# Kernel tuning notes

Measured on AMD Instinct MI355X. Metric: run time of the kernel, lower is better.

Reference implementation:

```python
import jax, jax.numpy as jnp
import numpy as np

B, R, L = 1024, 10, 512  # batch, num_rounds, lstm_size
EPS = 1e-10


def _gated(x, Wy, by, Wg, bg):
    # GatedTrans: tanh(Linear(x)) * sigmoid(Linear(x)); dropout is identity in eval
    return jnp.tanh(x @ Wy + by) * jax.nn.sigmoid(x @ Wg + bg)


def setup_inputs() -> dict:
    key = jax.random.key(0)
    ks = jax.random.split(key, 16)
    s_in = 1.0 / np.sqrt(2 * L)
    s_hid = 1.0 / np.sqrt(L)
    inp = {
        "hist": jax.random.normal(ks[0], (B, R, 2 * L), jnp.float32),
        "ques": jax.random.normal(ks[1], (B, R, 2 * L), jnp.float32),
        "noise": jax.random.uniform(ks[2], (B, R, R), jnp.float32),
        # H_embed GatedTrans params
        "Wy_h": jax.random.normal(ks[3], (2 * L, L), jnp.float32) * s_in,
        "by_h": jnp.zeros((L,), jnp.float32),
        "Wg_h": jax.random.normal(ks[4], (2 * L, L), jnp.float32) * s_in,
        "bg_h": jnp.zeros((L,), jnp.float32),
        # Q_embed GatedTrans params
        "Wy_q": jax.random.normal(ks[5], (2 * L, L), jnp.float32) * s_in,
        "by_q": jnp.zeros((L,), jnp.float32),
        "Wg_q": jax.random.normal(ks[6], (2 * L, L), jnp.float32) * s_in,
        "bg_q": jnp.zeros((L,), jnp.float32),
        # MLP: Linear(2L->L), Linear(L->1)
        "W1": jax.random.normal(ks[7], (2 * L, L), jnp.float32) * s_in,
        "b1": jnp.zeros((L,), jnp.float32),
        "W2": jax.random.normal(ks[8], (L, 1), jnp.float32) * s_hid,
        "b2": jnp.zeros((1,), jnp.float32),
        # att: Linear(2->1)
        "Wa": jax.random.normal(ks[9], (2, 1), jnp.float32) * 0.7,
        "ba": jnp.zeros((1,), jnp.float32),
    }
    return inp


def _forward(hist, ques, noise, Wy_h, by_h, Wg_h, bg_h, Wy_q, by_q, Wg_q, bg_q,
             W1, b1, W2, b2, Wa, ba):
    h = _gated(hist, Wy_h, by_h, Wg_h, bg_h)  # [B,R,L], indexed by j (history round)
    q = _gated(ques, Wy_q, by_q, Wg_q, bg_q)  # [B,R,L], indexed by i (question round)
    # MLP layer 1 on concat(h_j, q_i) without materializing the 2L concat:
    sh = h @ W1[:L] + b1            # [B,R,L] (j part + bias)
    sq = q @ W1[L:]                 # [B,R,L] (i part)
    hid = sq[:, :, None, :] + sh[:, None, :, :]  # [B,R(i),R(j),L]
    score = (hid @ W2 + b2)[..., 0]              # [B,R,R]
    # delta_t = cumsum over rows of lower-triangular ones
    tri = jnp.tril(jnp.ones((R, R), jnp.float32))
    delta_t = jnp.cumsum(tri, axis=0)            # [R,R]
    # att Linear(2->1) on concat(score, delta_t)
    logits = score * Wa[0, 0] + delta_t * Wa[1, 0] + ba[0]  # [B,R,R]
    # per-round Gumbel softmax over prefix [:i+1], vectorized with tril mask
    g = -jnp.log(EPS - jnp.log(noise + EPS))     # Gumbel(0,1) noise
    mask = tri.astype(bool)                       # [R,R], True for j<=i
    z = jnp.where(mask, logits + g, -1e9)
    y_soft = jax.nn.softmax(z, axis=-1)           # temperature = 1
    one_hot = jax.nn.one_hot(jnp.argmax(z, axis=-1), R, dtype=logits.dtype)
    # straight-through: value = one_hot, gradient flows through y_soft (valid cols only)
    y = one_hot + (y_soft - jax.lax.stop_gradient(y_soft)) * tri
    return y


def reference(hist, ques, noise, Wy_h, by_h, Wg_h, bg_h, Wy_q, by_q, Wg_q, bg_q,
              W1, b1, W2, b2, Wa, ba):
    return _forward(hist, ques, noise, Wy_h, by_h, Wg_h, bg_h, Wy_q, by_q,
                    Wg_q, bg_q, W1, b1, W2, b2, Wa, ba)
```

## Files before the change

### kernel.cpp

```cpp
#include <hip/hip_runtime.h>
#include <math.h>

typedef float f4 __attribute__((ext_vector_type(4)));
typedef float f32x4 __attribute__((ext_vector_type(4)));
typedef _Float16 h4 __attribute__((ext_vector_type(4)));
typedef _Float16 h8 __attribute__((ext_vector_type(8)));

#define NB 1024
#define NR 10
#define NL 512
#define NM (NB*NR)
#define NK (2*NL)

#define BIMG_OFF   131072ull
#define BIMG_EMBED 4194304ull
#define WS_NEED    (BIMG_OFF + 2ull*BIMG_EMBED)

#define SCALE_A 16.0f
#define SCALE_B 512.0f
#define INV_SCALE (1.0f/8192.0f)

__global__ __launch_bounds__(256) void k_init(float* __restrict__ t) {
    int i = blockIdx.x*256 + threadIdx.x;
    if (i < 2*NM) t[i] = 0.0f;
}

__global__ __launch_bounds__(256) void k_vcalc(const float* __restrict__ W1,
                                               const float* __restrict__ b1,
                                               const float* __restrict__ W2,
                                               const float* __restrict__ b2,
                                               float* __restrict__ vh,
                                               float* __restrict__ vq,
                                               float* __restrict__ cc) {
    int tid = blockIdx.x*256 + threadIdx.x;
    if (tid < 2*NL) {
        const float* row = W1 + (size_t)tid*NL;
        float s = 0.0f;
        #pragma unroll 4
        for (int k = 0; k < NL; ++k) s = fmaf(row[k], W2[k], s);
        if (tid < NL) vh[tid] = s; else vq[tid-NL] = s;
    } else if (tid == 2*NL) {
        float s = 0.0f;
        for (int k = 0; k < NL; ++k) s = fmaf(b1[k], W2[k], s);
        cc[0] = s + b2[0];
    }
}

__global__ __launch_bounds__(256) void k_wsplit(const float* __restrict__ Wy_h,
    const float* __restrict__ Wg_h, const float* __restrict__ Wy_q,
    const float* __restrict__ Wg_q, char* __restrict__ Bimg)
{
    const int nh = blockIdx.x;
    const int ks = blockIdx.y;
    const int mi = blockIdx.z;
    const float* W = (mi==0) ? Wy_h : (mi==1) ? Wg_h : (mi==2) ? Wy_q : Wg_q;
    const int emb = mi >> 1, nfb = (mi & 1) * 4;
    __shared__ float Ws[32][68];
    const int t = threadIdx.x;
    const int kl = t >> 4, nl4 = (t & 15) * 4;
    #pragma unroll
    for (int i = 0; i < 2; ++i) {
        f4 wv = *(const f4*)(W + (size_t)(ks*32 + kl + 16*i)*NL + nh*64 + nl4);
        *(f4*)&Ws[kl + 16*i][nl4] = wv;
    }
    __syncthreads();
    const int kg = t >> 6, nl = t & 63;
    h8 hi, lo;
    #pragma unroll
    for (int e8 = 0; e8 < 8; ++e8) {
        float x = Ws[kg*8 + e8][nl] * SCALE_B;
        _Float16 h = (_Float16)x;
        hi[e8] = h;
        lo[e8] = (_Float16)(x - (float)h);
    }
    const int nf  = nfb + (nl >> 4);
    const int l16 = (nl & 15) + 16*kg;
    char* p = Bimg + (size_t)emb*BIMG_EMBED
            + ((size_t)(nh*32 + ks)*2)*8192 + nf*1024 + l16*16;
    *(h8*)p = hi;
    *(h8*)(p + 8192) = lo;
}

__global__ __launch_bounds__(256, 2) void k_embed_mfma(
    const float* __restrict__ hist, const float* __restrict__ ques,
    const char* __restrict__ Bimg,
    const float* __restrict__ by_h, const float* __restrict__ bg_h,
    const float* __restrict__ by_q, const float* __restrict__ bg_q,
    const float* __restrict__ vv,
    float* __restrict__ tout)
{
    const int z = blockIdx.z;
    const float* X  = z ? ques : hist;
    const float* by = z ? by_q : by_h;
    const float* bg = z ? bg_q : bg_h;
    const float* v  = vv + z*NL;
    float* tptr = tout + (size_t)z*NM;
    const int nt = blockIdx.y;
    const char* Bt0 = Bimg + (size_t)z*BIMG_EMBED + (size_t)nt*32*16384;
    const int row0 = blockIdx.x * 128;

    __shared__ uint4 smem[2048];
    char* sA = (char*)smem;
    char* sB = sA + 16384;
    uint4* sB4 = smem + 1024;

    const int t = threadIdx.x;
    const int l = t & 63, w = t >> 6;
    const int wr = w >> 1, wc = w & 1;

    const int arow = t >> 3;
    const int ak4  = (t & 7) << 2;
    const int akg  = (t & 7) >> 1;
    const int ae0  = (t & 1) << 2;
    const float* Xp = X + (size_t)(row0 + arow)*NK + ak4;
    const int awb = ((arow >> 4) * 1024) + (((arow & 15) + 16*akg) * 16) + ae0*2;

    f32x4 acc[4][4];
    #pragma unroll
    for (int m = 0; m < 4; ++m)
      #pragma unroll
      for (int n = 0; n < 4; ++n) { f32x4 zz = {0.f,0.f,0.f,0.f}; acc[m][n] = zz; }

    for (int ks = 0; ks < 32; ++ks) {
        const int k0 = ks << 5;
        #pragma unroll
        for (int i = 0; i < 4; ++i) {
            f4 a = *(const f4*)(Xp + k0 + (size_t)i*32*NK);
            h4 hi, lo;
            #pragma unroll
            for (int j = 0; j < 4; ++j) {
                float xs = a[j] * SCALE_A;
                _Float16 h = (_Float16)xs;
                hi[j] = h;
                lo[j] = (_Float16)(xs - (float)h);
            }
            *(h4*)(sA +        awb + i*2048) = hi;
            *(h4*)(sA + 8192 + awb + i*2048) = lo;
        }
        const uint4* bt = (const uint4*)(Bt0 + (size_t)ks*16384);
        #pragma unroll
        for (int j = 0; j < 4; ++j) sB4[t + 256*j] = bt[t + 256*j];
        __syncthreads();
        h8 av[4][2], bv[4][2];
        #pragma unroll
        for (int m = 0; m < 4; ++m)
          #pragma unroll
          for (int s = 0; s < 2; ++s)
            av[m][s] = *(const h8*)(sA + s*8192 + (wr*4 + m)*1024 + l*16);
        #pragma unroll
        for (int fn = 0; fn < 4; ++fn) {
            const int nf = (fn < 2) ? (wc*2 + fn) : (4 + wc*2 + (fn - 2));
            #pragma unroll
            for (int s = 0; s < 2; ++s)
                bv[fn][s] = *(const h8*)(sB + s*8192 + nf*1024 + l*16);
        }
        #pragma unroll
        for (int m = 0; m < 4; ++m)
          #pragma unroll
          for (int fn = 0; fn < 4; ++fn) {
            acc[m][fn] = __builtin_amdgcn_mfma_f32_16x16x32_f16(av[m][0], bv[fn][0], acc[m][fn], 0, 0, 0);
            acc[m][fn] = __builtin_amdgcn_mfma_f32_16x16x32_f16(av[m][0], bv[fn][1], acc[m][fn], 0, 0, 0);
            acc[m][fn] = __builtin_amdgcn_mfma_f32_16x16x32_f16(av[m][1], bv[fn][0], acc[m][fn], 0, 0, 0);
          }
        __syncthreads();
    }

    const int coll = l & 15, rg = l >> 4;
    #pragma unroll
    for (int m = 0; m < 4; ++m) {
      #pragma unroll
      for (int r = 0; r < 4; ++r) {
        float ps = 0.0f;
        #pragma unroll
        for (int n = 0; n < 2; ++n) {
            const int c = nt*64 + wc*32 + n*16 + coll;
            float y = acc[m][n  ][r]*INV_SCALE + by[c];
            float g = acc[m][n+2][r]*INV_SCALE + bg[c];
            ps += v[c] * (tanhf(y) * (1.0f/(1.0f + expf(-g))));
        }
        ps += __shfl_xor(ps, 1);
        ps += __shfl_xor(ps, 2);
        ps += __shfl_xor(ps, 4);
        ps += __shfl_xor(ps, 8);
        if (coll == 0)
            atomicAdd(&tptr[row0 + wr*64 + m*16 + rg*4 + r], ps);
      }
    }
}

__global__ __launch_bounds__(256) void k_embed(const float* __restrict__ X,
    const float* __restrict__ Wy, const float* __restrict__ by,
    const float* __restrict__ Wg, const float* __restrict__ bg,
    const float* __restrict__ v, float* __restrict__ tout)
{
    __shared__ float As[32][68];
    __shared__ float Bys[32][64];
    __shared__ float Bgs[32][64];
    const int tid  = threadIdx.x;
    const int row0 = blockIdx.x * 64;
    const int c0   = blockIdx.y * 64;
    const int tx = tid & 15, ty = tid >> 4;
    float accy[4][4] = {};
    float accg[4][4] = {};
    const int arow = tid >> 3;
    const int ak   = (tid & 7) << 2;
    const int bk   = tid >> 4;
    const int bc   = (tid & 15) << 2;
    const float* Xp0 = X + (size_t)(row0 + arow)*NK + ak;
    const float* Xp1 = Xp0 + (size_t)32*NK;
    for (int k0 = 0; k0 < NK; k0 += 32) {
        f4 a0 = *(const f4*)(Xp0 + k0);
        f4 a1 = *(const f4*)(Xp1 + k0);
        f4 y0 = *(const f4*)&Wy[(size_t)(k0+bk   )*NL + c0 + bc];
        f4 y1 = *(const f4*)&Wy[(size_t)(k0+bk+16)*NL + c0 + bc];
        f4 g0 = *(const f4*)&Wg[(size_t)(k0+bk   )*NL + c0 + bc];
        f4 g1 = *(const f4*)&Wg[(size_t)(k0+bk+16)*NL + c0 + bc];
        #pragma unroll
        for (int j = 0; j < 4; ++j) {
            As[ak+j][arow]      = a0[j];
            As[ak+j][arow + 32] = a1[j];
        }
        *(f4*)&Bys[bk   ][bc] = y0;
        *(f4*)&Bys[bk+16][bc] = y1;
        *(f4*)&Bgs[bk   ][bc] = g0;
        *(f4*)&Bgs[bk+16][bc] = g1;
        __syncthreads();
        #pragma unroll
        for (int kk = 0; kk < 32; ++kk) {
            f4 a   = *(const f4*)&As [kk][ty<<2];
            f4 byv = *(const f4*)&Bys[kk][tx<<2];
            f4 bgv = *(const f4*)&Bgs[kk][tx<<2];
            #pragma unroll
            for (int rr = 0; rr < 4; ++rr)
                #pragma unroll
                for (int cc2 = 0; cc2 < 4; ++cc2) {
                    accy[rr][cc2] = fmaf(a[rr], byv[cc2], accy[rr][cc2]);
                    accg[rr][cc2] = fmaf(a[rr], bgv[cc2], accg[rr][cc2]);
                }
        }
        __syncthreads();
    }
    float rowsum[4] = {0.f, 0.f, 0.f, 0.f};
    #pragma unroll
    for (int rr = 0; rr < 4; ++rr)
        #pragma unroll
        for (int cc2 = 0; cc2 < 4; ++cc2) {
            int c = c0 + (tx<<2) + cc2;
            float xy = accy[rr][cc2] + by[c];
            float xg = accg[rr][cc2] + bg[c];
            float hv = tanhf(xy) * (1.0f / (1.0f + expf(-xg)));
            rowsum[rr] += v[c] * hv;
        }
    float* red = &As[0][0];
    #pragma unroll
    for (int rr = 0; rr < 4; ++rr) red[(ty*4 + rr)*16 + tx] = rowsum[rr];
    __syncthreads();
    if (tid < 64) {
        float s = 0.0f;
        #pragma unroll
        for (int t2 = 0; t2 < 16; ++t2) s += red[tid*16 + t2];
        atomicAdd(&tout[row0 + tid], s);
    }
}

__global__ __launch_bounds__(256) void k_final(const float* __restrict__ th,
    const float* __restrict__ tq, const float* __restrict__ cc,
    const float* __restrict__ noise, const float* __restrict__ Wa,
    const float* __restrict__ ba, float* __restrict__ out)
{
    int idx = blockIdx.x*256 + threadIdx.x;
    if (idx >= NM) return;
    int b = idx / NR, i = idx % NR;
    float wa0 = Wa[0], wa1 = Wa[1], bav = ba[0], c = cc[0];
    float ti = tq[idx];
    const float EPS = 1e-10f;
    float best = -3.0e38f; int am = 0;
    for (int j = 0; j < NR; ++j) {
        float zz;
        if (j <= i) {
            float n = noise[idx*NR + j];
            float g = -logf(EPS - logf(n + EPS));
            float score = ti + th[b*NR + j] + c;
            zz = score*wa0 + (float)(i - j + 1)*wa1 + bav + g;
        } else {
            zz = -1.0e9f;
        }
        if (zz > best) { best = zz; am = j; }
    }
    #pragma unroll
    for (int j = 0; j < NR; ++j) out[idx*NR + j] = (j == am) ? 1.0f : 0.0f;
}

extern "C" void kernel_launch(void* const* d_in, const int* in_sizes, int n_in,
                              void* d_out, int out_size, void* d_ws, size_t ws_size,
                              hipStream_t stream) {
    (void)in_sizes; (void)n_in; (void)out_size;
    const float* hist  = (const float*)d_in[0];
    const float* ques  = (const float*)d_in[1];
    const float* noise = (const float*)d_in[2];
    const float* Wy_h  = (const float*)d_in[3];
    const float* by_h  = (const float*)d_in[4];
    const float* Wg_h  = (const float*)d_in[5];
    const float* bg_h  = (const float*)d_in[6];
    const float* Wy_q  = (const float*)d_in[7];
    const float* by_q  = (const float*)d_in[8];
    const float* Wg_q  = (const float*)d_in[9];
    const float* bg_q  = (const float*)d_in[10];
    const float* W1    = (const float*)d_in[11];
    const float* b1    = (const float*)d_in[12];
    const float* W2    = (const float*)d_in[13];
    const float* b2    = (const float*)d_in[14];
    const float* Wa    = (const float*)d_in[15];
    const float* ba    = (const float*)d_in[16];
    float* out = (float*)d_out;

    float* ws     = (float*)d_ws;
    float* t_h    = ws;
    float* t_q    = ws + NM;
    float* v_h    = ws + 2*NM;
    float* v_q    = v_h + NL;
    float* cconst = v_q + NL;

    k_init<<<(2*NM + 255)/256, 256, 0, stream>>>(t_h);
    k_vcalc<<<5, 256, 0, stream>>>(W1, b1, W2, b2, v_h, v_q, cconst);

    if (ws_size >= WS_NEED) {
        char* Bimg = (char*)d_ws + BIMG_OFF;
        k_wsplit<<<dim3(8, 32, 4), 256, 0, stream>>>(Wy_h, Wg_h, Wy_q, Wg_q, Bimg);
        k_embed_mfma<<<dim3(80, 8, 2), 256, 0, stream>>>(hist, ques, Bimg,
            by_h, bg_h, by_q, bg_q, v_h, t_h);
    } else {
        dim3 g(NM/64, NL/64);
        k_embed<<<g, 256, 0, stream>>>(hist, Wy_h, by_h, Wg_h, bg_h, v_h, t_h);
        k_embed<<<g, 256, 0, stream>>>(ques, Wy_q, by_q, Wg_q, bg_q, v_q, t_q);
    }
    k_final<<<(NM + 255)/256, 256, 0, stream>>>(t_h, t_q, cconst, noise, Wa, ba, out);
}
```

Measured before the change: 319.7 us.

## Pre-split activations into fp16 hi/lo tiles and stream via global_load_lds

Adds a k_asplit pass that converts hist/ques once into pre-tiled fp16 hi/lo images, so the MFMA kernel no longer re-converts each A tile for every one of the 8 column blocks. The new GEMM kernel fills both A and B tiles in LDS with direct global-to-LDS loads. k_vcalc is replaced by a block-per-row reduction, and the zeroing kernel by a memset. The extra image pass costs additional memory traffic and workspace (about 84 MB) and runs only if the workspace is large enough. The fallback kernel also gets an XOR-swizzled A layout.

```diff
diff --git a/kernel.cpp b/kernel.cpp
--- a/kernel.cpp
+++ b/kernel.cpp
@@ -14,35 +14,40 @@
 
 #define BIMG_OFF   131072ull
 #define BIMG_EMBED 4194304ull
+#define AIMG_OFF   (BIMG_OFF + 2ull*BIMG_EMBED)
+#define AIMG_EMBED (80ull*32ull*16384ull)
 #define WS_NEED    (BIMG_OFF + 2ull*BIMG_EMBED)
+#define WS_NEED2   (AIMG_OFF + 2ull*AIMG_EMBED)
 
 #define SCALE_A 16.0f
 #define SCALE_B 512.0f
 #define INV_SCALE (1.0f/8192.0f)
 
-__global__ __launch_bounds__(256) void k_init(float* __restrict__ t) {
-    int i = blockIdx.x*256 + threadIdx.x;
-    if (i < 2*NM) t[i] = 0.0f;
-}
-
-__global__ __launch_bounds__(256) void k_vcalc(const float* __restrict__ W1,
-                                               const float* __restrict__ b1,
-                                               const float* __restrict__ W2,
-                                               const float* __restrict__ b2,
-                                               float* __restrict__ vh,
-                                               float* __restrict__ vq,
-                                               float* __restrict__ cc) {
-    int tid = blockIdx.x*256 + threadIdx.x;
-    if (tid < 2*NL) {
-        const float* row = W1 + (size_t)tid*NL;
-        float s = 0.0f;
-        #pragma unroll 4
-        for (int k = 0; k < NL; ++k) s = fmaf(row[k], W2[k], s);
-        if (tid < NL) vh[tid] = s; else vq[tid-NL] = s;
-    } else if (tid == 2*NL) {
-        float s = 0.0f;
-        for (int k = 0; k < NL; ++k) s = fmaf(b1[k], W2[k], s);
-        cc[0] = s + b2[0];
+__device__ __forceinline__ void gl_lds16(const void* g, void* s) {
+    __builtin_amdgcn_global_load_lds(
+        (const __attribute__((address_space(1))) unsigned int*)g,
+        (__attribute__((address_space(3))) unsigned int*)s, 16, 0, 0);
+}
+
+__global__ __launch_bounds__(256) void k_vcalc2(const float* __restrict__ W1,
+    const float* __restrict__ b1, const float* __restrict__ W2,
+    const float* __restrict__ b2, float* __restrict__ vh,
+    float* __restrict__ vq, float* __restrict__ cc)
+{
+    const int o = blockIdx.x;
+    const float* row = (o < 1024) ? (W1 + (size_t)o*NL) : b1;
+    const int t = threadIdx.x;
+    float s = fmaf(row[t], W2[t], row[t+256]*W2[t+256]);
+    #pragma unroll
+    for (int d = 1; d < 64; d <<= 1) s += __shfl_xor(s, d);
+    __shared__ float red[4];
+    if ((t & 63) == 0) red[t >> 6] = s;
+    __syncthreads();
+    if (t == 0) {
+        float tot = red[0] + red[1] + red[2] + red[3];
+        if (o < 512) vh[o] = tot;
+        else if (o < 1024) vq[o-512] = tot;
+        else cc[0] = tot + b2[0];
     }
 }
 
@@ -81,13 +86,126 @@
     *(h8*)(p + 8192) = lo;
 }
 
-__global__ __launch_bounds__(256, 2) void k_embed_mfma(
+__global__ __launch_bounds__(256) void k_asplit(const float* __restrict__ hist,
+    const float* __restrict__ ques, char* __restrict__ Aimg)
+{
+    const int rb = blockIdx.x, ks = blockIdx.y, z = blockIdx.z;
+    const float* X = z ? ques : hist;
+    char* dst = Aimg + (size_t)z*AIMG_EMBED + ((size_t)(rb*32 + ks))*16384;
+    const int t = threadIdx.x;
+    #pragma unroll
+    for (int i = 0; i < 2; ++i) {
+        const int m   = i*4 + (t >> 6);
+        const int row = m*16 + (t & 15);
+        const int kg  = (t >> 4) & 3;
+        const float* src = X + (size_t)(rb*128 + row)*NK + ks*32 + kg*8;
+        f4 a0 = *(const f4*)src;
+        f4 a1 = *(const f4*)(src + 4);
+        h8 hi, lo;
+        #pragma unroll
+        for (int j = 0; j < 4; ++j) {
+            float x0 = a0[j] * SCALE_A;
+            _Float16 h0 = (_Float16)x0;
+            hi[j] = h0; lo[j] = (_Float16)(x0 - (float)h0);
+            float x1 = a1[j] * SCALE_A;
+            _Float16 h1 = (_Float16)x1;
+            hi[4+j] = h1; lo[4+j] = (_Float16)(x1 - (float)h1);
+        }
+        *(h8*)(dst + i*4096 + t*16) = hi;
+        *(h8*)(dst + 8192 + i*4096 + t*16) = lo;
+    }
+}
+
+__global__ __launch_bounds__(256) void k_embed_mfma2(
+    const char* __restrict__ Aimg, const char* __restrict__ Bimg,
+    const float* __restrict__ by_h, const float* __restrict__ bg_h,
+    const float* __restrict__ by_q, const float* __restrict__ bg_q,
+    const float* __restrict__ vv, float* __restrict__ tout)
+{
+    const int z = blockIdx.z, nt = blockIdx.y, rb = blockIdx.x;
+    const float* by = z ? by_q : by_h;
+    const float* bg = z ? bg_q : bg_h;
+    const float* v  = vv + z*NL;
+    float* tptr = tout + (size_t)z*NM;
+    const char* At = Aimg + (size_t)z*AIMG_EMBED + ((size_t)rb*32)*16384;
+    const char* Bt = Bimg + (size_t)z*BIMG_EMBED + (size_t)nt*32*16384;
+
+    __shared__ char smem[32768];
+    char* sA = smem;
+    char* sB = smem + 16384;
+
+    const int t = threadIdx.x;
+    const int l = t & 63, w = t >> 6;
+    const int wr = w >> 1, wc = w & 1;
+
+    f32x4 acc[4][4];
+    #pragma unroll
+    for (int m = 0; m < 4; ++m)
+      #pragma unroll
+      for (int n = 0; n < 4; ++n) { f32x4 zz = {0.f,0.f,0.f,0.f}; acc[m][n] = zz; }
+
+    for (int ks = 0; ks < 32; ++ks) {
+        const char* ga = At + ks*16384 + w*4096 + l*16;
+        const char* gb = Bt + ks*16384 + w*4096 + l*16;
+        #pragma unroll
+        for (int j = 0; j < 4; ++j) {
+            gl_lds16(ga + j*1024, sA + w*4096 + j*1024);
+            gl_lds16(gb + j*1024, sB + w*4096 + j*1024);
+        }
+        __syncthreads();
+        h8 av[4][2], bv[4][2];
+        #pragma unroll
+        for (int m = 0; m < 4; ++m)
+          #pragma unroll
+          for (int s = 0; s < 2; ++s)
+            av[m][s] = *(const h8*)(sA + s*8192 + (wr*4 + m)*1024 + l*16);
+        #pragma unroll
+        for (int fn = 0; fn < 4; ++fn) {
+            const int nf = (fn < 2) ? (wc*2 + fn) : (4 + wc*2 + (fn - 2));
+            #pragma unroll
+            for (int s = 0; s < 2; ++s)
+                bv[fn][s] = *(const h8*)(sB + s*8192 + nf*1024 + l*16);
+        }
+        #pragma unroll
+        for (int m = 0; m < 4; ++m)
+          #pragma unroll
+          for (int fn = 0; fn < 4; ++fn) {
+            acc[m][fn] = __builtin_amdgcn_mfma_f32_16x16x32_f16(av[m][0], bv[fn][0], acc[m][fn], 0, 0, 0);
+            acc[m][fn] = __builtin_amdgcn_mfma_f32_16x16x32_f16(av[m][0], bv[fn][1], acc[m][fn], 0, 0, 0);
+            acc[m][fn] = __builtin_amdgcn_mfma_f32_16x16x32_f16(av[m][1], bv[fn][0], acc[m][fn], 0, 0, 0);
+          }
+        __syncthreads();
+    }
+
+    const int coll = l & 15, rg = l >> 4;
+    #pragma unroll
+    for (int m = 0; m < 4; ++m) {
+      #pragma unroll
+      for (int r = 0; r < 4; ++r) {
+        float ps = 0.0f;
+        #pragma unroll
+        for (int n = 0; n < 2; ++n) {
+            const int c = nt*64 + wc*32 + n*16 + coll;
+            float y = acc[m][n  ][r]*INV_SCALE + by[c];
+            float g = acc[m][n+2][r]*INV_SCALE + bg[c];
+            ps += v[c] * (tanhf(y) * (1.0f/(1.0f + expf(-g))));
+        }
+        ps += __shfl_xor(ps, 1);
+        ps += __shfl_xor(ps, 2);
+        ps += __shfl_xor(ps, 4);
+        ps += __shfl_xor(ps, 8);
+        if (coll == 0)
+            atomicAdd(&tptr[rb*128 + wr*64 + m*16 + rg*4 + r], ps);
+      }
+    }
+}
+
+__global__ __launch_bounds__(256) void k_embed_mfma(
     const float* __restrict__ hist, const float* __restrict__ ques,
     const char* __restrict__ Bimg,
     const float* __restrict__ by_h, const float* __restrict__ bg_h,
     const float* __restrict__ by_q, const float* __restrict__ bg_q,
-    const float* __restrict__ vv,
-    float* __restrict__ tout)
+    const float* __restrict__ vv, float* __restrict__ tout)
 {
     const int z = blockIdx.z;
     const float* X  = z ? ques : hist;
@@ -99,10 +217,9 @@
     const char* Bt0 = Bimg + (size_t)z*BIMG_EMBED + (size_t)nt*32*16384;
     const int row0 = blockIdx.x * 128;
 
-    __shared__ uint4 smem[2048];
-    char* sA = (char*)smem;
-    char* sB = sA + 16384;
-    uint4* sB4 = smem + 1024;
+    __shared__ char smem[32768];
+    char* sA = smem;
+    char* sB = smem + 16384;
 
     const int t = threadIdx.x;
     const int l = t & 63, w = t >> 6;
@@ -113,7 +230,8 @@
     const int akg  = (t & 7) >> 1;
     const int ae0  = (t & 1) << 2;
     const float* Xp = X + (size_t)(row0 + arow)*NK + ak4;
-    const int awb = ((arow >> 4) * 1024) + (((arow & 15) + 16*akg) * 16) + ae0*2;
+    const int awb = (((arow >> 4) * 1024) + (((arow & 15) + 16*akg) * 16) + ae0*2)
+                    ^ (akg << 5);
 
     f32x4 acc[4][4];
     #pragma unroll
@@ -137,16 +255,18 @@
             *(h4*)(sA +        awb + i*2048) = hi;
             *(h4*)(sA + 8192 + awb + i*2048) = lo;
         }
-        const uint4* bt = (const uint4*)(Bt0 + (size_t)ks*16384);
-        #pragma unroll
-        for (int j = 0; j < 4; ++j) sB4[t + 256*j] = bt[t + 256*j];
+        const char* gb = Bt0 + (size_t)ks*16384 + w*4096 + l*16;
+        #pragma unroll
+        for (int j = 0; j < 4; ++j)
+            gl_lds16(gb + j*1024, sB + w*4096 + j*1024);
         __syncthreads();
         h8 av[4][2], bv[4][2];
+        const int alsw = (l*16) ^ ((l & 48) << 1);
         #pragma unroll
         for (int m = 0; m < 4; ++m)
           #pragma unroll
           for (int s = 0; s < 2; ++s)
-            av[m][s] = *(const h8*)(sA + s*8192 + (wr*4 + m)*1024 + l*16);
+            av[m][s] = *(const h8*)(sA + s*8192 + (wr*4 + m)*1024 + alsw);
         #pragma unroll
         for (int fn = 0; fn < 4; ++fn) {
             const int nf = (fn < 2) ? (wc*2 + fn) : (4 + wc*2 + (fn - 2));
@@ -321,10 +441,17 @@
     float* v_q    = v_h + NL;
     float* cconst = v_q + NL;
 
-    k_init<<<(2*NM + 255)/256, 256, 0, stream>>>(t_h);
-    k_vcalc<<<5, 256, 0, stream>>>(W1, b1, W2, b2, v_h, v_q, cconst);
-
-    if (ws_size >= WS_NEED) {
+    hipMemsetAsync(t_h, 0, 2*NM*sizeof(float), stream);
+    k_vcalc2<<<1025, 256, 0, stream>>>(W1, b1, W2, b2, v_h, v_q, cconst);
+
+    if (ws_size >= WS_NEED2) {
+        char* Bimg = (char*)d_ws + BIMG_OFF;
+        char* Aimg = (char*)d_ws + AIMG_OFF;
+        k_wsplit<<<dim3(8, 32, 4), 256, 0, stream>>>(Wy_h, Wg_h, Wy_q, Wg_q, Bimg);
+        k_asplit<<<dim3(80, 32, 2), 256, 0, stream>>>(hist, ques, Aimg);
+        k_embed_mfma2<<<dim3(80, 8, 2), 256, 0, stream>>>(Aimg, Bimg,
+            by_h, bg_h, by_q, bg_q, v_h, t_h);
+    } else if (ws_size >= WS_NEED) {
         char* Bimg = (char*)d_ws + BIMG_OFF;
         k_wsplit<<<dim3(8, 32, 4), 256, 0, stream>>>(Wy_h, Wg_h, Wy_q, Wg_q, Bimg);
         k_embed_mfma<<<dim3(80, 8, 2), 256, 0, stream>>>(hist, ques, Bimg,
```

Measured after the change: 314.4 us. About the same (-1.7%).

## Pre-split activations to fp16 image and double-buffer MFMA GEMM via global_load_lds

Applied to the files above, without the earlier changes.

A new prep kernel folds the zero-init, v-vector reduction, weight split and a new activation split (fp32 to hi/lo fp16 in MFMA-ready layout) into one launch. The GEMM kernel then streams both A and B tiles straight into LDS with global_load_lds, double-buffered with manual waitcnt and barriers, and raises wave priority around the MFMA block. This removes per-tile fp32 conversion and register round-trips from the GEMM inner loop and cuts launch count. In exchange, the activation image (about 80MB of extra writes and reads) goes through global memory and needs a larger workspace.

```diff
diff --git a/kernel.cpp b/kernel.cpp
--- a/kernel.cpp
+++ b/kernel.cpp
@@ -14,133 +14,157 @@
 
 #define BIMG_OFF   131072ull
 #define BIMG_EMBED 4194304ull
-#define WS_NEED    (BIMG_OFF + 2ull*BIMG_EMBED)
+#define AIMG_OFF   (BIMG_OFF + 2ull*BIMG_EMBED)
+#define AIMG_EMBED (80ull*32ull*16384ull)
+#define WS_NEED2   (AIMG_OFF + 2ull*AIMG_EMBED)
 
 #define SCALE_A 16.0f
 #define SCALE_B 512.0f
 #define INV_SCALE (1.0f/8192.0f)
 
-__global__ __launch_bounds__(256) void k_init(float* __restrict__ t) {
-    int i = blockIdx.x*256 + threadIdx.x;
-    if (i < 2*NM) t[i] = 0.0f;
-}
-
-__global__ __launch_bounds__(256) void k_vcalc(const float* __restrict__ W1,
-                                               const float* __restrict__ b1,
-                                               const float* __restrict__ W2,
-                                               const float* __restrict__ b2,
-                                               float* __restrict__ vh,
-                                               float* __restrict__ vq,
-                                               float* __restrict__ cc) {
-    int tid = blockIdx.x*256 + threadIdx.x;
-    if (tid < 2*NL) {
-        const float* row = W1 + (size_t)tid*NL;
-        float s = 0.0f;
-        #pragma unroll 4
-        for (int k = 0; k < NL; ++k) s = fmaf(row[k], W2[k], s);
-        if (tid < NL) vh[tid] = s; else vq[tid-NL] = s;
-    } else if (tid == 2*NL) {
-        float s = 0.0f;
-        for (int k = 0; k < NL; ++k) s = fmaf(b1[k], W2[k], s);
-        cc[0] = s + b2[0];
-    }
-}
-
-__global__ __launch_bounds__(256) void k_wsplit(const float* __restrict__ Wy_h,
-    const float* __restrict__ Wg_h, const float* __restrict__ Wy_q,
-    const float* __restrict__ Wg_q, char* __restrict__ Bimg)
-{
-    const int nh = blockIdx.x;
-    const int ks = blockIdx.y;
-    const int mi = blockIdx.z;
-    const float* W = (mi==0) ? Wy_h : (mi==1) ? Wg_h : (mi==2) ? Wy_q : Wg_q;
-    const int emb = mi >> 1, nfb = (mi & 1) * 4;
+__device__ __forceinline__ void gl_lds16(const void* g, void* s) {
+    __builtin_amdgcn_global_load_lds(
+        (const __attribute__((address_space(1))) unsigned int*)g,
+        (__attribute__((address_space(3))) unsigned int*)s, 16, 0, 0);
+}
+
+__global__ __launch_bounds__(256) void k_prep(
+    const float* __restrict__ hist, const float* __restrict__ ques,
+    const float* __restrict__ Wy_h, const float* __restrict__ Wg_h,
+    const float* __restrict__ Wy_q, const float* __restrict__ Wg_q,
+    const float* __restrict__ W1, const float* __restrict__ b1,
+    const float* __restrict__ W2, const float* __restrict__ b2,
+    char* __restrict__ Aimg, char* __restrict__ Bimg,
+    float* __restrict__ vh, float* __restrict__ vq, float* __restrict__ cc,
+    float* __restrict__ tzero)
+{
     __shared__ float Ws[32][68];
+    __shared__ float red[4];
+    const int bid = blockIdx.x;
     const int t = threadIdx.x;
-    const int kl = t >> 4, nl4 = (t & 15) * 4;
-    #pragma unroll
-    for (int i = 0; i < 2; ++i) {
-        f4 wv = *(const f4*)(W + (size_t)(ks*32 + kl + 16*i)*NL + nh*64 + nl4);
-        *(f4*)&Ws[kl + 16*i][nl4] = wv;
-    }
-    __syncthreads();
-    const int kg = t >> 6, nl = t & 63;
-    h8 hi, lo;
-    #pragma unroll
-    for (int e8 = 0; e8 < 8; ++e8) {
-        float x = Ws[kg*8 + e8][nl] * SCALE_B;
-        _Float16 h = (_Float16)x;
-        hi[e8] = h;
-        lo[e8] = (_Float16)(x - (float)h);
-    }
-    const int nf  = nfb + (nl >> 4);
-    const int l16 = (nl & 15) + 16*kg;
-    char* p = Bimg + (size_t)emb*BIMG_EMBED
-            + ((size_t)(nh*32 + ks)*2)*8192 + nf*1024 + l16*16;
-    *(h8*)p = hi;
-    *(h8*)(p + 8192) = lo;
-}
-
-__global__ __launch_bounds__(256, 2) void k_embed_mfma(
-    const float* __restrict__ hist, const float* __restrict__ ques,
-    const char* __restrict__ Bimg,
+
+    if (bid < 5120) {
+        const int rb = bid % 80, ks = (bid / 80) % 32, z = bid / 2560;
+        const float* X = z ? ques : hist;
+        char* dst = Aimg + (size_t)z*AIMG_EMBED + ((size_t)(rb*32 + ks))*16384;
+        #pragma unroll
+        for (int i = 0; i < 2; ++i) {
+            const int m   = i*4 + (t >> 6);
+            const int row = m*16 + (t & 15);
+            const int kg  = (t >> 4) & 3;
+            const float* src = X + (size_t)(rb*128 + row)*NK + ks*32 + kg*8;
+            f4 a0 = *(const f4*)src;
+            f4 a1 = *(const f4*)(src + 4);
+            h8 hi, lo;
+            #pragma unroll
+            for (int j = 0; j < 4; ++j) {
+                float x0 = a0[j] * SCALE_A;
+                _Float16 h0 = (_Float16)x0;
+                hi[j] = h0; lo[j] = (_Float16)(x0 - (float)h0);
+                float x1 = a1[j] * SCALE_A;
+                _Float16 h1 = (_Float16)x1;
+                hi[4+j] = h1; lo[4+j] = (_Float16)(x1 - (float)h1);
+            }
+            *(h8*)(dst + i*4096 + t*16) = hi;
+            *(h8*)(dst + 8192 + i*4096 + t*16) = lo;
+        }
+    } else if (bid < 6144) {
+        const int wb = bid - 5120;
+        const int nh = wb % 8, ks = (wb / 8) % 32, mi = wb / 256;
+        const float* W = (mi==0) ? Wy_h : (mi==1) ? Wg_h : (mi==2) ? Wy_q : Wg_q;
+        const int emb = mi >> 1, nfb = (mi & 1) * 4;
+        const int kl = t >> 4, nl4 = (t & 15) * 4;
+        #pragma unroll
+        for (int i = 0; i < 2; ++i) {
+            f4 wv = *(const f4*)(W + (size_t)(ks*32 + kl + 16*i)*NL + nh*64 + nl4);
+            *(f4*)&Ws[kl + 16*i][nl4] = wv;
+        }
+        __syncthreads();
+        const int kg = t >> 6, nl = t & 63;
+        h8 hi, lo;
+        #pragma unroll
+        for (int e8 = 0; e8 < 8; ++e8) {
+            float x = Ws[kg*8 + e8][nl] * SCALE_B;
+            _Float16 h = (_Float16)x;
+            hi[e8] = h;
+            lo[e8] = (_Float16)(x - (float)h);
+        }
+        const int nf  = nfb + (nl >> 4);
+        const int l16 = (nl & 15) + 16*kg;
+        char* p = Bimg + (size_t)emb*BIMG_EMBED
+                + ((size_t)(nh*32 + ks)*2)*8192 + nf*1024 + l16*16;
+        *(h8*)p = hi;
+        *(h8*)(p + 8192) = lo;
+    } else if (bid < 7169) {
+        const int o = bid - 6144;
+        const float* row = (o < 1024) ? (W1 + (size_t)o*NL) : b1;
+        float s = fmaf(row[t], W2[t], row[t+256]*W2[t+256]);
+        #pragma unroll
+        for (int d = 1; d < 64; d <<= 1) s += __shfl_xor(s, d);
+        if ((t & 63) == 0) red[t >> 6] = s;
+        __syncthreads();
+        if (t == 0) {
+            float tot = red[0] + red[1] + red[2] + red[3];
+            if (o < 512) vh[o] = tot;
+            else if (o < 1024) vq[o-512] = tot;
+            else cc[0] = tot + b2[0];
+        }
+    } else {
+        const int zb = bid - 7169;
+        f4 zz = {0.f, 0.f, 0.f, 0.f};
+        *(f4*)(tzero + (size_t)zb*1024 + t*4) = zz;
+    }
+}
+
+__global__ __launch_bounds__(256, 2) void k_embed_mfma3(
+    const char* __restrict__ Aimg, const char* __restrict__ Bimg,
     const float* __restrict__ by_h, const float* __restrict__ bg_h,
     const float* __restrict__ by_q, const float* __restrict__ bg_q,
-    const float* __restrict__ vv,
-    float* __restrict__ tout)
-{
-    const int z = blockIdx.z;
-    const float* X  = z ? ques : hist;
+    const float* __restrict__ vv, float* __restrict__ tout)
+{
+    const int z = blockIdx.z, nt = blockIdx.y, rb = blockIdx.x;
     const float* by = z ? by_q : by_h;
     const float* bg = z ? bg_q : bg_h;
     const float* v  = vv + z*NL;
     float* tptr = tout + (size_t)z*NM;
-    const int nt = blockIdx.y;
-    const char* Bt0 = Bimg + (size_t)z*BIMG_EMBED + (size_t)nt*32*16384;
-    const int row0 = blockIdx.x * 128;
-
-    __shared__ uint4 smem[2048];
-    char* sA = (char*)smem;
-    char* sB = sA + 16384;
-    uint4* sB4 = smem + 1024;
+    const char* At = Aimg + (size_t)z*AIMG_EMBED + ((size_t)rb*32)*16384;
+    const char* Bt = Bimg + (size_t)z*BIMG_EMBED + (size_t)nt*32*16384;
+
+    __shared__ char smem[65536];
 
     const int t = threadIdx.x;
     const int l = t & 63, w = t >> 6;
     const int wr = w >> 1, wc = w & 1;
 
-    const int arow = t >> 3;
-    const int ak4  = (t & 7) << 2;
-    const int akg  = (t & 7) >> 1;
-    const int ae0  = (t & 1) << 2;
-    const float* Xp = X + (size_t)(row0 + arow)*NK + ak4;
-    const int awb = ((arow >> 4) * 1024) + (((arow & 15) + 16*akg) * 16) + ae0*2;
-
     f32x4 acc[4][4];
     #pragma unroll
     for (int m = 0; m < 4; ++m)
       #pragma unroll
       for (int n = 0; n < 4; ++n) { f32x4 zz = {0.f,0.f,0.f,0.f}; acc[m][n] = zz; }
 
+    auto stage = [&](int b, int ksrc) {
+        const char* ga = At + (size_t)ksrc*16384 + w*4096 + l*16;
+        const char* gb = Bt + (size_t)ksrc*16384 + w*4096 + l*16;
+        char* da = smem + b*32768 + w*4096;
+        char* db = smem + b*32768 + 16384 + w*4096;
+        #pragma unroll
+        for (int j = 0; j < 4; ++j) {
+            gl_lds16(ga + j*1024, da + j*1024);
+            gl_lds16(gb + j*1024, db + j*1024);
+        }
+    };
+
+    stage(0, 0);
+    stage(1, 1);
+    asm volatile("s_waitcnt vmcnt(8)" ::: "memory");
+    __builtin_amdgcn_s_barrier();
+
+    #pragma unroll 2
     for (int ks = 0; ks < 32; ++ks) {
-        const int k0 = ks << 5;
-        #pragma unroll
-        for (int i = 0; i < 4; ++i) {
-            f4 a = *(const f4*)(Xp + k0 + (size_t)i*32*NK);
-            h4 hi, lo;
-            #pragma unroll
-            for (int j = 0; j < 4; ++j) {
-                float xs = a[j] * SCALE_A;
-                _Float16 h = (_Float16)xs;
-                hi[j] = h;
-                lo[j] = (_Float16)(xs - (float)h);
-            }
-            *(h4*)(sA +        awb + i*2048) = hi;
-            *(h4*)(sA + 8192 + awb + i*2048) = lo;
-        }
-        const uint4* bt = (const uint4*)(Bt0 + (size_t)ks*16384);
-        #pragma unroll
-        for (int j = 0; j < 4; ++j) sB4[t + 256*j] = bt[t + 256*j];
-        __syncthreads();
+        const int cur = ks & 1;
+        const char* sA = smem + cur*32768;
+        const char* sB = sA + 16384;
+
         h8 av[4][2], bv[4][2];
         #pragma unroll
         for (int m = 0; m < 4; ++m)
@@ -154,6 +178,12 @@
             for (int s = 0; s < 2; ++s)
                 bv[fn][s] = *(const h8*)(sB + s*8192 + nf*1024 + l*16);
         }
+        asm volatile("s_waitcnt lgkmcnt(0)" ::: "memory");
+        __builtin_amdgcn_sched_barrier(0);
+        __builtin_amdgcn_s_barrier();
+        if (ks + 2 < 32) stage(cur, ks + 2);
+
+        __builtin_amdgcn_s_setprio(1);
         #pragma unroll
         for (int m = 0; m < 4; ++m)
           #pragma unroll
@@ -162,7 +192,11 @@
             acc[m][fn] = __builtin_amdgcn_mfma_f32_16x16x32_f16(av[m][0], bv[fn][1], acc[m][fn], 0, 0, 0);
             acc[m][fn] = __builtin_amdgcn_mfma_f32_16x16x32_f16(av[m][1], bv[fn][0], acc[m][fn], 0, 0, 0);
           }
-        __syncthreads();
+        __builtin_amdgcn_s_setprio(0);
+
+        if (ks < 30)       asm volatile("s_waitcnt vmcnt(8)" ::: "memory");
+        else if (ks == 30) asm volatile("s_waitcnt vmcnt(0)" ::: "memory");
+        if (ks < 31) __builtin_amdgcn_s_barrier();
     }
 
     const int coll = l & 15, rg = l >> 4;
@@ -183,8 +217,30 @@
         ps += __shfl_xor(ps, 4);
         ps += __shfl_xor(ps, 8);
         if (coll == 0)
-            atomicAdd(&tptr[row0 + wr*64 + m*16 + rg*4 + r], ps);
+            atomicAdd(&tptr[rb*128 + wr*64 + m*16 + rg*4 + r], ps);
       }
+    }
+}
+
+__global__ __launch_bounds__(256) void k_vcalc2(const float* __restrict__ W1,
+    const float* __restrict__ b1, const float* __restrict__ W2,
+    const float* __restrict__ b2, float* __restrict__ vh,
+    float* __restrict__ vq, float* __restrict__ cc)
+{
+    const int o = blockIdx.x;
+    const float* row = (o < 1024) ? (W1 + (size_t)o*NL) : b1;
+    const int t = threadIdx.x;
+    float s = fmaf(row[t], W2[t], row[t+256]*W2[t+256]);
+    #pragma unroll
+    for (int d = 1; d < 64; d <<= 1) s += __shfl_xor(s, d);
+    __shared__ float red[4];
+    if ((t & 63) == 0) red[t >> 6] = s;
+    __syncthreads();
+    if (t == 0) {
+        float tot = red[0] + red[1] + red[2] + red[3];
+        if (o < 512) vh[o] = tot;
+        else if (o < 1024) vq[o-512] = tot;
+        else cc[0] = tot + b2[0];
     }
 }
 
@@ -321,15 +377,16 @@
     float* v_q    = v_h + NL;
     float* cconst = v_q + NL;
 
-    k_init<<<(2*NM + 255)/256, 256, 0, stream>>>(t_h);
-    k_vcalc<<<5, 256, 0, stream>>>(W1, b1, W2, b2, v_h, v_q, cconst);
-
-    if (ws_size >= WS_NEED) {
+    if (ws_size >= WS_NEED2) {
         char* Bimg = (char*)d_ws + BIMG_OFF;
-        k_wsplit<<<dim3(8, 32, 4), 256, 0, stream>>>(Wy_h, Wg_h, Wy_q, Wg_q, Bimg);
-        k_embed_mfma<<<dim3(80, 8, 2), 256, 0, stream>>>(hist, ques, Bimg,
+        char* Aimg = (char*)d_ws + AIMG_OFF;
+        k_prep<<<7189, 256, 0, stream>>>(hist, ques, Wy_h, Wg_h, Wy_q, Wg_q,
+            W1, b1, W2, b2, Aimg, Bimg, v_h, v_q, cconst, t_h);
+        k_embed_mfma3<<<dim3(80, 8, 2), 256, 0, stream>>>(Aimg, Bimg,
             by_h, bg_h, by_q, bg_q, v_h, t_h);
     } else {
+        hipMemsetAsync(t_h, 0, 2*NM*sizeof(float), stream);
+        k_vcalc2<<<1025, 256, 0, stream>>>(W1, b1, W2, b2, v_h, v_q, cconst);
         dim3 g(NM/64, NL/64);
         k_embed<<<g, 256, 0, stream>>>(hist, Wy_h, by_h, Wg_h, bg_h, v_h, t_h);
         k_embed<<<g, 256, 0, stream>>>(ques, Wy_q, by_q, Wg_q, bg_q, v_q, t_q);
```

After: 277.7 us. 1.15x faster.
